# Performance work log

Measured on AMD Instinct MI355X. Metric: run time of the kernel, lower is better.

Reference implementation:

```python
import jax, jax.numpy as jnp
import numpy as np

N_NODES = 100000


def gcn_conv(x, edge_index, W, b):
    # PyG GCNConv: add self-loops, symmetric normalization D^-1/2 (A+I) D^-1/2, then X W + b
    n = x.shape[0]
    loop = jnp.arange(n, dtype=edge_index.dtype)
    src = jnp.concatenate([edge_index[0], loop])
    dst = jnp.concatenate([edge_index[1], loop])
    deg = jax.ops.segment_sum(jnp.ones_like(dst, dtype=x.dtype), dst, num_segments=n)
    dinv = jnp.where(deg > 0, jax.lax.rsqrt(deg), 0.0).astype(x.dtype)
    norm = dinv[src] * dinv[dst]            # [E+n]
    h = x @ W                               # [n, out] project first (out <= in)
    msg = h[src] * norm[:, None]            # [E+n, out] edge messages
    out = jax.ops.segment_sum(msg, dst, num_segments=n)
    return out + b


def setup_inputs() -> dict:
    key = jax.random.key(0)
    ks = jax.random.split(key, 8)
    E = 3200000
    x = jax.random.normal(ks[0], (N_NODES, 128), dtype=jnp.float32)
    edge_index = jax.random.randint(ks[1], (2, E), 0, N_NODES, dtype=jnp.int64)
    W1 = jax.random.normal(ks[2], (128, 32), dtype=jnp.float32) * (1.0 / np.sqrt(128))
    b1 = jnp.zeros((32,), dtype=jnp.float32)
    W2 = jax.random.normal(ks[3], (32, 16), dtype=jnp.float32) * (1.0 / np.sqrt(32))
    b2 = jnp.zeros((16,), dtype=jnp.float32)
    Wl = jax.random.normal(ks[4], (16, 1), dtype=jnp.float32) * (1.0 / np.sqrt(16))
    bl = jnp.zeros((1,), dtype=jnp.float32)
    return {"x": x, "edge_index": edge_index, "W1": W1, "b1": b1,
            "W2": W2, "b2": b2, "Wl": Wl, "bl": bl}


def reference(x, edge_index, W1, b1, W2, b2, Wl, bl):
    h = jax.nn.relu(gcn_conv(x, edge_index, W1, b1))   # [N, 32]
    h = jax.nn.relu(gcn_conv(h, edge_index, W2, b2))   # [N, 16]
    return h @ Wl + bl                                  # [N, 1]
```

## Files before the change

kernel.cpp:

```cpp
#include <hip/hip_runtime.h>
#include <stdint.h>


#define TPB 256
#define NBLK 512
#define BKT_SHIFT 10
#define BKT_NODES 1024
#define MAXBKT 128
#define SRC_BITS 17
#define SRC_MASK 0x1FFFF

__device__ __forceinline__ int edge_at(const int* __restrict__ e, long long idx, int is64) {
    return e[is64 ? (2 * idx) : idx];
}

#define DETECT_IS64(edges)                                            \
    __shared__ int s_is64;                                            \
    if (threadIdx.x < 64) {                                           \
        int v_ = (edges)[2 * threadIdx.x + 1];                        \
        unsigned long long m_ = __ballot(v_ != 0);                    \
        if (threadIdx.x == 0) s_is64 = (m_ == 0ULL) ? 1 : 0;          \
    }

__device__ __forceinline__ void f4add(float4& a, const float4 b) {
    a.x += b.x; a.y += b.y; a.z += b.z; a.w += b.w;
}

__global__ void k_hist(const int* __restrict__ edges, int* __restrict__ hist,
                       long long E, int nbkt) {
    __shared__ int cnt[MAXBKT];
    DETECT_IS64(edges);
    if (threadIdx.x < nbkt) cnt[threadIdx.x] = 0;
    __syncthreads();
    const int is64 = s_is64;
    const long long chunk = (E + NBLK - 1) / NBLK;
    const long long beg = (long long)blockIdx.x * chunk;
    const long long end = (beg + chunk < E) ? beg + chunk : E;
    for (long long e = beg + threadIdx.x; e < end; e += blockDim.x) {
        int d = edge_at(edges, E + e, is64);
        atomicAdd(&cnt[d >> BKT_SHIFT], 1);
    }
    __syncthreads();
    if (threadIdx.x < nbkt) hist[threadIdx.x * NBLK + blockIdx.x] = cnt[threadIdx.x];
}

__global__ void k_reorder(const int* __restrict__ edges, const int* __restrict__ histoff,
                          unsigned int* __restrict__ tmp, long long E, int nbkt) {
    __shared__ int off[MAXBKT];
    DETECT_IS64(edges);
    if (threadIdx.x < nbkt) off[threadIdx.x] = histoff[threadIdx.x * NBLK + blockIdx.x];
    __syncthreads();
    const int is64 = s_is64;
    const long long chunk = (E + NBLK - 1) / NBLK;
    const long long beg = (long long)blockIdx.x * chunk;
    const long long end = (beg + chunk < E) ? beg + chunk : E;
    for (long long e = beg + threadIdx.x; e < end; e += blockDim.x) {
        int s = edge_at(edges, e, is64);
        int d = edge_at(edges, E + e, is64);
        int pos = atomicAdd(&off[d >> BKT_SHIFT], 1);
        tmp[pos] = ((unsigned int)(d & (BKT_NODES - 1)) << SRC_BITS) | (unsigned int)s;
    }
}

__global__ void k_scan_partial(const int* __restrict__ cnt, int* __restrict__ partial, int N) {
    __shared__ int lds[TPB];
    int i = blockIdx.x * TPB + threadIdx.x;
    lds[threadIdx.x] = (i < N) ? cnt[i] : 0;
    __syncthreads();
    for (int s = TPB / 2; s > 0; s >>= 1) {
        if (threadIdx.x < s) lds[threadIdx.x] += lds[threadIdx.x + s];
        __syncthreads();
    }
    if (threadIdx.x == 0) partial[blockIdx.x] = lds[0];
}

__global__ void k_scan_top(int* __restrict__ partial, int NB) {
    __shared__ int lds[512];
    int t = threadIdx.x;
    int v = (t < NB) ? partial[t] : 0;
    lds[t] = v;
    __syncthreads();
    for (int off = 1; off < 512; off <<= 1) {
        int x = (t >= off) ? lds[t - off] : 0;
        __syncthreads();
        lds[t] += x;
        __syncthreads();
    }
    if (t < NB) partial[t] = lds[t] - v;
    if (t == 0) partial[NB] = lds[511];
}

__global__ void k_scan_write(const int* __restrict__ cnt, const int* __restrict__ partial,
                             int* __restrict__ outp, int N, int NB) {
    __shared__ int lds[TPB];
    int i = blockIdx.x * TPB + threadIdx.x;
    int v = (i < N) ? cnt[i] : 0;
    lds[threadIdx.x] = v;
    __syncthreads();
    for (int off = 1; off < TPB; off <<= 1) {
        int x = (threadIdx.x >= off) ? lds[threadIdx.x - off] : 0;
        __syncthreads();
        lds[threadIdx.x] += x;
        __syncthreads();
    }
    if (i < N) outp[i] = partial[blockIdx.x] + lds[threadIdx.x] - v;
    if (i == N) outp[N] = partial[NB];
}

__global__ void k_sortbucket(const unsigned int* __restrict__ tmp, const int* __restrict__ histoff,
                             float* __restrict__ dinv, int* __restrict__ row_ptr,
                             int* __restrict__ col, int N, long long E, int nbkt) {
    __shared__ int scnt[BKT_NODES];
    const int t = threadIdx.x;
    const int b = blockIdx.x;
    const int begI = histoff[b * NBLK];
    const int endI = histoff[(b + 1) * NBLK];
    scnt[t] = 0; scnt[t + 512] = 0;
    __syncthreads();
    for (int e = begI + t; e < endI; e += 512)
        atomicAdd(&scnt[tmp[e] >> SRC_BITS], 1);
    __syncthreads();
    const int c0 = scnt[t], c1 = scnt[t + 512];
    for (int off = 1; off < BKT_NODES; off <<= 1) {
        int i0 = t, i1 = t + 512;
        int a0 = (i0 >= off) ? scnt[i0 - off] : 0;
        int a1 = (i1 >= off) ? scnt[i1 - off] : 0;
        __syncthreads();
        scnt[i0] += a0; scnt[i1] += a1;
        __syncthreads();
    }
    const int rp0 = begI + scnt[t] - c0;
    const int rp1 = begI + scnt[t + 512] - c1;
    const int v0 = (b << BKT_SHIFT) + t;
    const int v1 = v0 + 512;
    if (v0 < N) { dinv[v0] = rsqrtf((float)(c0 + 1)); row_ptr[v0] = rp0; }
    if (v1 < N) { dinv[v1] = rsqrtf((float)(c1 + 1)); row_ptr[v1] = rp1; }
    if (b == nbkt - 1 && t == 0) row_ptr[N] = (int)E;
    __syncthreads();
    scnt[t] = rp0; scnt[t + 512] = rp1;
    __syncthreads();
    for (int e = begI + t; e < endI; e += 512) {
        unsigned int p = tmp[e];
        int pos = atomicAdd(&scnt[p >> SRC_BITS], 1);
        col[pos] = (int)(p & SRC_MASK);
    }
}

__global__ void k_proj1(const float* __restrict__ x, const float* __restrict__ W1,
                        const float* __restrict__ dinv, float* __restrict__ h1s, int N) {
    __shared__ float w[128 * 32];
    for (int i = threadIdx.x; i < 128 * 32; i += TPB) w[i] = W1[i];
    __syncthreads();
    int t = blockIdx.x * TPB + threadIdx.x;
    int v = t >> 5, f = t & 31;
    if (v >= N) return;
    const float4* xr = (const float4*)(x + (long long)v * 128);
    float acc = 0.f;
#pragma unroll
    for (int k4 = 0; k4 < 32; k4++) {
        float4 xv = xr[k4];
        int k = k4 * 4;
        acc = fmaf(xv.x, w[(k + 0) * 32 + f], acc);
        acc = fmaf(xv.y, w[(k + 1) * 32 + f], acc);
        acc = fmaf(xv.z, w[(k + 2) * 32 + f], acc);
        acc = fmaf(xv.w, w[(k + 3) * 32 + f], acc);
    }
    h1s[(long long)v * 32 + f] = acc * dinv[v];
}

__global__ void k_gather1(const float* __restrict__ h1s, const int* __restrict__ col,
                          const int* __restrict__ rp, const float* __restrict__ dinv,
                          const float* __restrict__ b1, float* __restrict__ out1, int N) {
    int t = blockIdx.x * TPB + threadIdx.x;
    int v = t >> 5;
    if (v >= N) return;
    int l32 = threadIdx.x & 31;
    int slot = l32 >> 3;
    int f4 = l32 & 7;
    int beg = rp[v], end = rp[v + 1];
    float4 s0 = make_float4(0.f, 0.f, 0.f, 0.f);
    float4 s1 = make_float4(0.f, 0.f, 0.f, 0.f);
    if (slot == 0)
        s0 = *(const float4*)(h1s + (long long)v * 32 + f4 * 4);
    int i = beg + slot;
    for (; i + 4 < end; i += 8) {
        int u0 = col[i], u1 = col[i + 4];
        float4 a = *(const float4*)(h1s + (long long)u0 * 32 + f4 * 4);
        float4 b = *(const float4*)(h1s + (long long)u1 * 32 + f4 * 4);
        f4add(s0, a);
        f4add(s1, b);
    }
    if (i < end) {
        int u0 = col[i];
        float4 a = *(const float4*)(h1s + (long long)u0 * 32 + f4 * 4);
        f4add(s0, a);
    }
    f4add(s0, s1);
    s0.x += __shfl_xor(s0.x, 8);  s0.y += __shfl_xor(s0.y, 8);
    s0.z += __shfl_xor(s0.z, 8);  s0.w += __shfl_xor(s0.w, 8);
    s0.x += __shfl_xor(s0.x, 16); s0.y += __shfl_xor(s0.y, 16);
    s0.z += __shfl_xor(s0.z, 16); s0.w += __shfl_xor(s0.w, 16);
    if (slot == 0) {
        float dv = dinv[v];
        float4 bb = *(const float4*)(b1 + f4 * 4);
        float4 r;
        r.x = dv * s0.x + bb.x; r.x = r.x > 0.f ? r.x : 0.f;
        r.y = dv * s0.y + bb.y; r.y = r.y > 0.f ? r.y : 0.f;
        r.z = dv * s0.z + bb.z; r.z = r.z > 0.f ? r.z : 0.f;
        r.w = dv * s0.w + bb.w; r.w = r.w > 0.f ? r.w : 0.f;
        *(float4*)(out1 + (long long)v * 32 + f4 * 4) = r;
    }
}

__global__ void k_proj2(const float* __restrict__ out1, const float* __restrict__ W2,
                        const float* __restrict__ dinv, float* __restrict__ h2s, int N) {
    __shared__ float w[32 * 16];
    for (int i = threadIdx.x; i < 32 * 16; i += TPB) w[i] = W2[i];
    __syncthreads();
    int t = blockIdx.x * TPB + threadIdx.x;
    int v = t >> 4, f = t & 15;
    if (v >= N) return;
    const float4* xr = (const float4*)(out1 + (long long)v * 32);
    float acc = 0.f;
#pragma unroll
    for (int k4 = 0; k4 < 8; k4++) {
        float4 xv = xr[k4];
        int k = k4 * 4;
        acc = fmaf(xv.x, w[(k + 0) * 16 + f], acc);
        acc = fmaf(xv.y, w[(k + 1) * 16 + f], acc);
        acc = fmaf(xv.z, w[(k + 2) * 16 + f], acc);
        acc = fmaf(xv.w, w[(k + 3) * 16 + f], acc);
    }
    h2s[(long long)v * 16 + f] = acc * dinv[v];
}

__global__ void k_gather2(const float* __restrict__ h2s, const int* __restrict__ col,
                          const int* __restrict__ rp, const float* __restrict__ dinv,
                          const float* __restrict__ b2, const float* __restrict__ Wl,
                          const float* __restrict__ bl, float* __restrict__ out, int N) {
    int t = blockIdx.x * TPB + threadIdx.x;
    int v = t >> 5;
    if (v >= N) return;
    int l32 = threadIdx.x & 31;
    int slot = l32 >> 2;
    int f4 = l32 & 3;
    int beg = rp[v], end = rp[v + 1];
    float4 s = make_float4(0.f, 0.f, 0.f, 0.f);
    if (slot == 0)
        s = *(const float4*)(h2s + (long long)v * 16 + f4 * 4);
    for (int i = beg + slot; i < end; i += 8) {
        int u = col[i];
        float4 a = *(const float4*)(h2s + (long long)u * 16 + f4 * 4);
        f4add(s, a);
    }
    s.x += __shfl_xor(s.x, 4);  s.y += __shfl_xor(s.y, 4);
    s.z += __shfl_xor(s.z, 4);  s.w += __shfl_xor(s.w, 4);
    s.x += __shfl_xor(s.x, 8);  s.y += __shfl_xor(s.y, 8);
    s.z += __shfl_xor(s.z, 8);  s.w += __shfl_xor(s.w, 8);
    s.x += __shfl_xor(s.x, 16); s.y += __shfl_xor(s.y, 16);
    s.z += __shfl_xor(s.z, 16); s.w += __shfl_xor(s.w, 16);
    if (slot == 0) {
        float dv = dinv[v];
        float4 bb = *(const float4*)(b2 + f4 * 4);
        float4 wl = *(const float4*)(Wl + f4 * 4);
        float rx = dv * s.x + bb.x; rx = rx > 0.f ? rx : 0.f;
        float ry = dv * s.y + bb.y; ry = ry > 0.f ? ry : 0.f;
        float rz = dv * s.z + bb.z; rz = rz > 0.f ? rz : 0.f;
        float rw = dv * s.w + bb.w; rw = rw > 0.f ? rw : 0.f;
        float p = rx * wl.x + ry * wl.y + rz * wl.z + rw * wl.w;
        p += __shfl_xor(p, 1);
        p += __shfl_xor(p, 2);
        if (f4 == 0) out[v] = p + bl[0];
    }
}

extern "C" void kernel_launch(void* const* d_in, const int* in_sizes, int n_in,
                              void* d_out, int out_size, void* d_ws, size_t ws_size,
                              hipStream_t stream) {
    const float* x    = (const float*)d_in[0];
    const int*   edges= (const int*)d_in[1];
    const float* W1   = (const float*)d_in[2];
    const float* b1   = (const float*)d_in[3];
    const float* W2   = (const float*)d_in[4];
    const float* b2   = (const float*)d_in[5];
    const float* Wl   = (const float*)d_in[6];
    const float* bl   = (const float*)d_in[7];
    float* out = (float*)d_out;

    const int       N = in_sizes[0] / 128;
    const long long E = (long long)in_sizes[1] / 2;
    const int    nbkt = (N + BKT_NODES - 1) >> BKT_SHIFT;
    const int      NH = nbkt * NBLK;
    const int    NB_H = (NH + TPB - 1) / TPB;

    char* ws = (char*)d_ws;
    size_t off = 0;
    auto carve = [&](size_t bytes) { void* p = ws + off; off = (off + bytes + 255) & ~(size_t)255; return p; };
    float* dinv    = (float*)carve((size_t)N * 4);
    int*   row_ptr = (int*)  carve((size_t)(N + 1) * 4);
    int*   partialH= (int*)  carve((size_t)(NB_H + 1) * 4);
    int*   hist    = (int*)  carve((size_t)NH * 4);
    int*   histoff = (int*)  carve((size_t)(NH + 1) * 4);
    int*   col     = (int*)  carve((size_t)E * 4);
    float* unionA  = (float*)carve((size_t)N * 64 * 4);
    float* h2s     = (float*)carve((size_t)N * 16 * 4);
    (void)ws_size;

    float*        h1s  = unionA;
    float*        out1 = unionA + (size_t)N * 32;
    unsigned int* tmp  = (unsigned int*)unionA;

    hipLaunchKernelGGL(k_hist, dim3(NBLK), dim3(TPB), 0, stream, edges, hist, E, nbkt);
    hipLaunchKernelGGL(k_scan_partial, dim3(NB_H), dim3(TPB), 0, stream, hist, partialH, NH);
    hipLaunchKernelGGL(k_scan_top, dim3(1), dim3(512), 0, stream, partialH, NB_H);
    hipLaunchKernelGGL(k_scan_write, dim3(NB_H + 1), dim3(TPB), 0, stream, hist, partialH, histoff, NH, NB_H);
    hipLaunchKernelGGL(k_reorder, dim3(NBLK), dim3(TPB), 0, stream, edges, histoff, tmp, E, nbkt);
    hipLaunchKernelGGL(k_sortbucket, dim3(nbkt), dim3(512), 0, stream, tmp, histoff, dinv, row_ptr, col, N, E, nbkt);
    hipLaunchKernelGGL(k_proj1, dim3((N * 32 + TPB - 1) / TPB), dim3(TPB), 0, stream, x, W1, dinv, h1s, N);
    hipLaunchKernelGGL(k_gather1, dim3((N * 32 + TPB - 1) / TPB), dim3(TPB), 0, stream, h1s, col, row_ptr, dinv, b1, out1, N);
    hipLaunchKernelGGL(k_proj2, dim3((N * 16 + TPB - 1) / TPB), dim3(TPB), 0, stream, out1, W2, dinv, h2s, N);
    hipLaunchKernelGGL(k_gather2, dim3((N * 32 + TPB - 1) / TPB), dim3(TPB), 0, stream, h2s, col, row_ptr, dinv, b2, Wl, bl, out, N);
}
```

Before: 357.0 us.

## Restructure projection kernels to stage node rows in shared memory with register-tiled outputs

Both dense projection kernels now stage a tile of 64 node rows in XOR-swizzled shared memory instead of staging the weights there. Each wavefront owns a contiguous block of output columns, and each thread computes 8 (or 4) outputs per node. Weights are read as wave-uniform scalar loads via readfirstlane. This replaces redundant per-output-column reads of each x row from global memory and per-scalar LDS weight reads, at the cost of more registers and a larger LDS footprint per block.

```diff
diff --git a/kernel.cpp b/kernel.cpp
--- a/kernel.cpp
+++ b/kernel.cpp
@@ -146,26 +146,46 @@
     }
 }
 
-__global__ void k_proj1(const float* __restrict__ x, const float* __restrict__ W1,
-                        const float* __restrict__ dinv, float* __restrict__ h1s, int N) {
-    __shared__ float w[128 * 32];
-    for (int i = threadIdx.x; i < 128 * 32; i += TPB) w[i] = W1[i];
-    __syncthreads();
-    int t = blockIdx.x * TPB + threadIdx.x;
-    int v = t >> 5, f = t & 31;
-    if (v >= N) return;
-    const float4* xr = (const float4*)(x + (long long)v * 128);
-    float acc = 0.f;
+__global__ __launch_bounds__(TPB) void k_proj1(const float* __restrict__ x,
+                        const float* __restrict__ W1, const float* __restrict__ dinv,
+                        float* __restrict__ h1s, int N) {
+    __shared__ float4 xs[64 * 32];
+    const int t = threadIdx.x;
+    const int vbase = blockIdx.x * 64;
+    for (int idx = t; idx < 64 * 32; idx += TPB) {
+        int v = idx >> 5, k4 = idx & 31;
+        int vg = vbase + v;
+        float4 val = (vg < N) ? *(const float4*)(x + (long long)vg * 128 + k4 * 4)
+                              : make_float4(0.f, 0.f, 0.f, 0.f);
+        xs[v * 32 + (k4 ^ (v & 31))] = val;
+    }
+    __syncthreads();
+    const int l = t & 63;
+    const int cb = __builtin_amdgcn_readfirstlane((t >> 6) * 8);
+    float acc[8] = {0.f, 0.f, 0.f, 0.f, 0.f, 0.f, 0.f, 0.f};
+#pragma unroll 4
+    for (int k4 = 0; k4 < 32; k4++) {
+        float4 xv = xs[l * 32 + (k4 ^ (l & 31))];
 #pragma unroll
-    for (int k4 = 0; k4 < 32; k4++) {
-        float4 xv = xr[k4];
-        int k = k4 * 4;
-        acc = fmaf(xv.x, w[(k + 0) * 32 + f], acc);
-        acc = fmaf(xv.y, w[(k + 1) * 32 + f], acc);
-        acc = fmaf(xv.z, w[(k + 2) * 32 + f], acc);
-        acc = fmaf(xv.w, w[(k + 3) * 32 + f], acc);
-    }
-    h1s[(long long)v * 32 + f] = acc * dinv[v];
+        for (int j = 0; j < 4; j++) {
+            const float* wr = W1 + (k4 * 4 + j) * 32 + cb;
+            float4 wa = *(const float4*)(wr);
+            float4 wb = *(const float4*)(wr + 4);
+            float xj = (j == 0) ? xv.x : (j == 1) ? xv.y : (j == 2) ? xv.z : xv.w;
+            acc[0] = fmaf(xj, wa.x, acc[0]); acc[1] = fmaf(xj, wa.y, acc[1]);
+            acc[2] = fmaf(xj, wa.z, acc[2]); acc[3] = fmaf(xj, wa.w, acc[3]);
+            acc[4] = fmaf(xj, wb.x, acc[4]); acc[5] = fmaf(xj, wb.y, acc[5]);
+            acc[6] = fmaf(xj, wb.z, acc[6]); acc[7] = fmaf(xj, wb.w, acc[7]);
+        }
+    }
+    const int v = vbase + l;
+    if (v < N) {
+        float dv = dinv[v];
+        *(float4*)(h1s + (long long)v * 32 + cb) =
+            make_float4(acc[0] * dv, acc[1] * dv, acc[2] * dv, acc[3] * dv);
+        *(float4*)(h1s + (long long)v * 32 + cb + 4) =
+            make_float4(acc[4] * dv, acc[5] * dv, acc[6] * dv, acc[7] * dv);
+    }
 }
 
 __global__ void k_gather1(const float* __restrict__ h1s, const int* __restrict__ col,
@@ -212,26 +232,40 @@
     }
 }
 
-__global__ void k_proj2(const float* __restrict__ out1, const float* __restrict__ W2,
-                        const float* __restrict__ dinv, float* __restrict__ h2s, int N) {
-    __shared__ float w[32 * 16];
-    for (int i = threadIdx.x; i < 32 * 16; i += TPB) w[i] = W2[i];
-    __syncthreads();
-    int t = blockIdx.x * TPB + threadIdx.x;
-    int v = t >> 4, f = t & 15;
-    if (v >= N) return;
-    const float4* xr = (const float4*)(out1 + (long long)v * 32);
-    float acc = 0.f;
+__global__ __launch_bounds__(TPB) void k_proj2(const float* __restrict__ out1,
+                        const float* __restrict__ W2, const float* __restrict__ dinv,
+                        float* __restrict__ h2s, int N) {
+    __shared__ float4 xs[64 * 8];
+    const int t = threadIdx.x;
+    const int vbase = blockIdx.x * 64;
+    for (int idx = t; idx < 64 * 8; idx += TPB) {
+        int v = idx >> 3, k4 = idx & 7;
+        int vg = vbase + v;
+        float4 val = (vg < N) ? *(const float4*)(out1 + (long long)vg * 32 + k4 * 4)
+                              : make_float4(0.f, 0.f, 0.f, 0.f);
+        xs[v * 8 + (k4 ^ (v & 7))] = val;
+    }
+    __syncthreads();
+    const int l = t & 63;
+    const int cb = __builtin_amdgcn_readfirstlane((t >> 6) * 4);
+    float acc[4] = {0.f, 0.f, 0.f, 0.f};
 #pragma unroll
     for (int k4 = 0; k4 < 8; k4++) {
-        float4 xv = xr[k4];
-        int k = k4 * 4;
-        acc = fmaf(xv.x, w[(k + 0) * 16 + f], acc);
-        acc = fmaf(xv.y, w[(k + 1) * 16 + f], acc);
-        acc = fmaf(xv.z, w[(k + 2) * 16 + f], acc);
-        acc = fmaf(xv.w, w[(k + 3) * 16 + f], acc);
-    }
-    h2s[(long long)v * 16 + f] = acc * dinv[v];
+        float4 xv = xs[l * 8 + (k4 ^ (l & 7))];
+#pragma unroll
+        for (int j = 0; j < 4; j++) {
+            float4 w4 = *(const float4*)(W2 + (k4 * 4 + j) * 16 + cb);
+            float xj = (j == 0) ? xv.x : (j == 1) ? xv.y : (j == 2) ? xv.z : xv.w;
+            acc[0] = fmaf(xj, w4.x, acc[0]); acc[1] = fmaf(xj, w4.y, acc[1]);
+            acc[2] = fmaf(xj, w4.z, acc[2]); acc[3] = fmaf(xj, w4.w, acc[3]);
+        }
+    }
+    const int v = vbase + l;
+    if (v < N) {
+        float dv = dinv[v];
+        *(float4*)(h2s + (long long)v * 16 + cb) =
+            make_float4(acc[0] * dv, acc[1] * dv, acc[2] * dv, acc[3] * dv);
+    }
 }
 
 __global__ void k_gather2(const float* __restrict__ h2s, const int* __restrict__ col,
@@ -316,8 +350,8 @@
     hipLaunchKernelGGL(k_scan_write, dim3(NB_H + 1), dim3(TPB), 0, stream, hist, partialH, histoff, NH, NB_H);
     hipLaunchKernelGGL(k_reorder, dim3(NBLK), dim3(TPB), 0, stream, edges, histoff, tmp, E, nbkt);
     hipLaunchKernelGGL(k_sortbucket, dim3(nbkt), dim3(512), 0, stream, tmp, histoff, dinv, row_ptr, col, N, E, nbkt);
-    hipLaunchKernelGGL(k_proj1, dim3((N * 32 + TPB - 1) / TPB), dim3(TPB), 0, stream, x, W1, dinv, h1s, N);
+    hipLaunchKernelGGL(k_proj1, dim3((N + 63) / 64), dim3(TPB), 0, stream, x, W1, dinv, h1s, N);
     hipLaunchKernelGGL(k_gather1, dim3((N * 32 + TPB - 1) / TPB), dim3(TPB), 0, stream, h1s, col, row_ptr, dinv, b1, out1, N);
-    hipLaunchKernelGGL(k_proj2, dim3((N * 16 + TPB - 1) / TPB), dim3(TPB), 0, stream, out1, W2, dinv, h2s, N);
+    hipLaunchKernelGGL(k_proj2, dim3((N + 63) / 64), dim3(TPB), 0, stream, out1, W2, dinv, h2s, N);
     hipLaunchKernelGGL(k_gather2, dim3((N * 32 + TPB - 1) / TPB), dim3(TPB), 0, stream, h2s, col, row_ptr, dinv, b2, Wl, bl, out, N);
 }
```

New measurement: 312.1 us. 12.6% less time.
